# Performance work log

Hardware: AMD Instinct MI355X
Metric: run time of the kernel (lower is better)

Reference implementation:

```python
import jax, jax.numpy as jnp
import numpy as np

LAMB = 0.05
ITERS = 3
EPS = 1e-6


def _l2norm(x):
    return x / jnp.linalg.norm(x, axis=-1, keepdims=True)


def setup_inputs() -> dict:
    key = jax.random.key(0)
    k1, k2, k3, k4 = jax.random.split(key, 4)
    Bi, Bt, R, W, D = 128, 128, 36, 50, 1024
    # region / word features, L2-normalized so fg_sims are cosine similarities
    imgs = _l2norm(jax.random.normal(k1, (Bi, R, D), dtype=jnp.float32))
    caps = _l2norm(jax.random.normal(k2, (Bt, W, D), dtype=jnp.float32))
    # valid lengths; force max so static shapes R, W match int(lens.max())
    img_lens = jax.random.randint(k3, (Bi,), 10, R + 1).astype(jnp.int32)
    img_lens = img_lens.at[0].set(R)
    cap_lens = jax.random.randint(k4, (Bt,), 5, W + 1).astype(jnp.int32)
    cap_lens = cap_lens.at[0].set(W)
    return {"imgs": imgs, "caps": caps, "img_lens": img_lens, "cap_lens": cap_lens}


def _forward(imgs, caps, img_lens, cap_lens):
    Bi, R, D = imgs.shape
    Bt, W, _ = caps.shape
    # fine-grained similarities: [Bi, Bt, R, W]
    fg_sims = jnp.einsum('ird,cwd->icrw', imgs, caps)
    # fine-grained validity mask from lengths
    img_m = (jnp.arange(R)[None, :] < img_lens[:, None])          # [Bi, R]
    cap_m = (jnp.arange(W)[None, :] < cap_lens[:, None])          # [Bt, W]
    mask = (img_m[:, None, :, None] & cap_m[None, :, None, :])    # [Bi, Bt, R, W] bool
    maskf = mask.astype(fg_sims.dtype)

    # _ave_init: uniform marginals over valid rows / cols
    rmask = img_m[:, None, :].astype(fg_sims.dtype) * jnp.ones((1, Bt, 1), fg_sims.dtype)
    r = rmask / rmask.sum(axis=-1, keepdims=True)                 # [Bi, Bt, R]
    cmask = cap_m[None, :, :].astype(fg_sims.dtype) * jnp.ones((Bi, 1, 1), fg_sims.dtype)
    c = cmask / cmask.sum(axis=-1, keepdims=True)                 # [Bi, Bt, W]

    # Sinkhorn-Knopp on cost (1 - fg_sims), masked entries get cost +inf -> P=0
    P = jnp.where(mask, jnp.exp(-(1.0 - fg_sims) / LAMB), 0.0)
    P = P / (P.sum(axis=(-2, -1), keepdims=True) + EPS)
    for _ in range(ITERS):
        u = P.sum(axis=-1) + EPS                                  # [Bi, Bt, R]
        P = P * (r / u)[..., None]
        v = P.sum(axis=-2) + EPS                                  # [Bi, Bt, W]
        P = P * (c / v)[..., None, :]

    sims = (fg_sims * P * maskf).sum(axis=(-2, -1))               # [Bi, Bt]
    return sims


def reference(imgs, caps, img_lens, cap_lens):
    return _forward(imgs, caps, img_lens, cap_lens)
```

## Files before the change

### kernel.cpp

```cpp
#include <hip/hip_runtime.h>
#include <stdint.h>

#define BI 128
#define BT 128
#define RR 36
#define WW 50
#define DD 1024
#define NN 6400
#define SEPS 1e-6f
#define L2E20 28.853900817779268f

typedef __attribute__((ext_vector_type(8))) short short8v;
typedef __attribute__((ext_vector_type(4))) float float4v;
typedef __attribute__((ext_vector_type(2))) unsigned int uint2v;

__device__ __forceinline__ unsigned short f2bf(float f){
  unsigned u = __float_as_uint(f);
  return (unsigned short)((u + 0x7FFFu + ((u >> 16) & 1u)) >> 16);
}

template<int CTRL>
__device__ __forceinline__ int dpp_addi(int x){
  int y = __builtin_amdgcn_mov_dpp(x, CTRL, 0xF, 0xF, true);
  return x + y;
}
__device__ __forceinline__ int iwaveSum(int x){
  x = dpp_addi<0x121>(x);
  x = dpp_addi<0x122>(x);
  x = dpp_addi<0x124>(x);
  x = dpp_addi<0x128>(x);
  {
    uint2v r = __builtin_amdgcn_permlane16_swap((unsigned)x, (unsigned)x, false, false);
    x = (int)r[0] + (int)r[1];
  }
  {
    uint2v r = __builtin_amdgcn_permlane32_swap((unsigned)x, (unsigned)x, false, false);
    x = (int)r[0] + (int)r[1];
  }
  return x;
}
__device__ __forceinline__ int maskedSum128(const int* __restrict__ v,
                                            int lim, int lane){
  const int a = v[2 * lane];
  const int b = v[2 * lane + 1];
  int s = ((2 * lane) < lim ? a : 0) + ((2 * lane + 1) < lim ? b : 0);
  return iwaveSum(s);
}

__global__ __launch_bounds__(256) void gather_cvt_kernel(
    const float* __restrict__ imgs, const float* __restrict__ caps,
    const int* __restrict__ il, const int* __restrict__ cl,
    unsigned short* __restrict__ Ab, unsigned short* __restrict__ Bb,
    int* __restrict__ rowoff, int* __restrict__ coloff){
  const int b = blockIdx.x;
  const int t = threadIdx.x;
  const int lane = t & 63;
  if (b < BI * RR){
    const int i = b / RR, r = b % RR;
    if (r >= il[i]) return;
    const int ro = maskedSum128(il, i, lane);
    if (r == 0 && t == 0) rowoff[i] = ro;
    const float4 v = *(const float4*)(imgs + (size_t)b * DD + t * 4);
    ushort4 o = make_ushort4(f2bf(v.x), f2bf(v.y), f2bf(v.z), f2bf(v.w));
    *(ushort4*)(Ab + (size_t)(ro + r) * DD + t * 4) = o;
  } else {
    const int bb = b - BI * RR;
    const int c = bb / WW, w = bb % WW;
    if (w >= cl[c]) return;
    const int co = maskedSum128(cl, c, lane);
    if (w == 0 && t == 0) coloff[c] = co;
    const float4 v = *(const float4*)(caps + (size_t)bb * DD + t * 4);
    ushort4 o = make_ushort4(f2bf(v.x), f2bf(v.y), f2bf(v.z), f2bf(v.w));
    *(ushort4*)(Bb + (size_t)(co + w) * DD + t * 4) = o;
  }
}

__global__ __launch_bounds__(256) void gemm_kernel(
    const unsigned short* __restrict__ A, const unsigned short* __restrict__ B,
    const int* __restrict__ il, const int* __restrict__ cl,
    float* __restrict__ C){
  __shared__ __align__(16) unsigned char LDS[49152];
  const int tid = threadIdx.x;
  const int lane = tid & 63, wv = tid >> 6;
  const int Mp = __builtin_amdgcn_readfirstlane(maskedSum128(il, BI, lane));
  const int Np = __builtin_amdgcn_readfirstlane(maskedSum128(cl, BT, lane));
  const int nnb = (Np + 127) >> 7;
  const int nact = ((Mp + 127) >> 7) * nnb;
  const int bx = blockIdx.x;
  if (bx >= nact) return;
  const int mb = bx / nnb, nb = bx - mb * nnb;
  const int m0 = mb * 128, n0 = nb * 128;

  const int l15 = lane & 15, lhi = lane >> 4;
  const int wr = wv >> 1, wc = wv & 1;

  const unsigned short* sp[4];
  #pragma unroll
  for (int j = 0; j < 4; j++){
    const int u = j * 256 + tid;
    const int v = u & 511;
    const int sup = v >> 3, slot = v & 7;
    const int sub = slot ^ (sup & 7);
    const int row = sup * 2 + (sub >> 2);
    const int kg  = sub & 3;
    sp[j] = ((u < 512) ? (A + (size_t)(m0 + row) * DD)
                       : (B + (size_t)(n0 + row) * DD)) + kg * 8;
  }

  float4v acc[4][4];
  #pragma unroll
  for (int a1 = 0; a1 < 4; a1++)
    #pragma unroll
    for (int b1 = 0; b1 < 4; b1++)
      acc[a1][b1] = (float4v){0.f, 0.f, 0.f, 0.f};

#define STAGE(BUF, CH) { \
    _Pragma("unroll") \
    for (int j = 0; j < 4; j++) \
      __builtin_amdgcn_global_load_lds( \
          (const __attribute__((address_space(1))) void*)(sp[j] + (CH) * 32), \
          (__attribute__((address_space(3))) void*)(LDS + (BUF) * 16384 + (j * 256 + tid) * 16), \
          16, 0, 0); }

#define LUNIT(row) (((row) >> 1) * 8 + (((((row) & 1) << 2) + lhi) ^ (((row) >> 1) & 7)))

#define COMPUTE(BUF) { \
    short8v af[4], bf[4]; \
    _Pragma("unroll") \
    for (int tr = 0; tr < 4; tr++){ \
      const int row = wr * 64 + tr * 16 + l15; \
      af[tr] = *(const short8v*)(LDS + (BUF) * 16384 + LUNIT(row) * 16); \
    } \
    _Pragma("unroll") \
    for (int tw = 0; tw < 4; tw++){ \
      const int row = wc * 64 + tw * 16 + l15; \
      bf[tw] = *(const short8v*)(LDS + (BUF) * 16384 + 8192 + LUNIT(row) * 16); \
    } \
    _Pragma("unroll") \
    for (int tr = 0; tr < 4; tr++) \
      _Pragma("unroll") \
      for (int tw = 0; tw < 4; tw++) \
        acc[tr][tw] = __builtin_amdgcn_mfma_f32_16x16x32_bf16( \
            af[tr], bf[tw], acc[tr][tw], 0, 0, 0); }

#define WAIT8  asm volatile("s_waitcnt vmcnt(8)" ::: "memory")
#define WAIT4  asm volatile("s_waitcnt vmcnt(4)" ::: "memory")
#define WAIT0  asm volatile("s_waitcnt vmcnt(0)" ::: "memory")
#define BAR    __builtin_amdgcn_s_barrier()

  STAGE(0, 0);
  STAGE(1, 1);
  #pragma unroll 1
  for (int k = 0; k < 10; k++){
    const int c = 3 * k;
    STAGE(2, c + 2); WAIT8; BAR; COMPUTE(0); BAR;
    STAGE(0, c + 3); WAIT8; BAR; COMPUTE(1); BAR;
    STAGE(1, c + 4); WAIT8; BAR; COMPUTE(2); BAR;
  }
  WAIT4; BAR; COMPUTE(0); BAR;
  WAIT0; BAR; COMPUTE(1);

#undef STAGE
#undef LUNIT
#undef COMPUTE
#undef WAIT8
#undef WAIT4
#undef WAIT0
#undef BAR

  #pragma unroll
  for (int tr = 0; tr < 4; tr++)
    #pragma unroll
    for (int tw = 0; tw < 4; tw++)
      #pragma unroll
      for (int j = 0; j < 4; j++){
        int m = m0 + wr * 64 + tr * 16 + lhi * 4 + j;
        int n = n0 + wc * 64 + tw * 16 + l15;
        C[(size_t)m * NN + n] = acc[tr][tw][j];
      }
}

template<int CTRL>
__device__ __forceinline__ float dpp_add(float x){
  int y = __builtin_amdgcn_mov_dpp(__float_as_int(x), CTRL, 0xF, 0xF, true);
  return x + __int_as_float(y);
}
__device__ __forceinline__ float q16sum(float x){
  x = dpp_add<0x121>(x);
  x = dpp_add<0x122>(x);
  x = dpp_add<0x124>(x);
  x = dpp_add<0x128>(x);
  return x;
}
__device__ __forceinline__ float pl16comb(float x){
  unsigned xi = __float_as_uint(x);
  uint2v r = __builtin_amdgcn_permlane16_swap(xi, xi, false, false);
  return __uint_as_float(r[0]) + __uint_as_float(r[1]);
}
__device__ __forceinline__ float pl32comb(float x){
  unsigned xi = __float_as_uint(x);
  uint2v r = __builtin_amdgcn_permlane32_swap(xi, xi, false, false);
  return __uint_as_float(r[0]) + __uint_as_float(r[1]);
}

__global__ __launch_bounds__(256) void sink_kernel(
    const float* __restrict__ fg, const int* __restrict__ il,
    const int* __restrict__ cl, const int* __restrict__ rowoff,
    const int* __restrict__ coloff, float* __restrict__ out){
  const int lane = threadIdx.x & 63;
  const int gw = blockIdx.x * 4 + (threadIdx.x >> 6);
  const int i = gw >> 7, c = gw & 127;
  const int q = lane >> 4, t = lane & 15;

  const int ilen = __builtin_amdgcn_readfirstlane(il[i]);
  const int clen = __builtin_amdgcn_readfirstlane(cl[c]);
  const int ro   = __builtin_amdgcn_readfirstlane(rowoff[i]);
  const int co   = __builtin_amdgcn_readfirstlane(coloff[c]);
  const float* base = fg + (size_t)ro * NN + co;
  const float inv_il = __fdividef(1.0f, (float)ilen);
  const float inv_cl = __fdividef(1.0f, (float)clen);
  const bool v0 = (t      < clen);
  const bool v1 = (t + 16 < clen);
  const bool v2 = (t + 32 < clen);
  const bool v3 = (t + 48 < clen);
  const int r0 = 9 * q;
  const int off0 = r0 * NN + t;

  float p0[9], p1[9], p2[9], p3[9];
  float ts = 0.f;
  #pragma unroll
  for (int k = 0; k < 9; k++){
    const bool rv = (r0 + k) < ilen;
    const float a0 = base[off0 + k * NN];
    const float a1 = base[off0 + k * NN + 16];
    const float a2 = base[off0 + k * NN + 32];
    const float a3 = base[off0 + k * NN + 48];
    p0[k] = (rv && v0) ? exp2f(fmaf(a0, L2E20, -L2E20)) : 0.f;
    p1[k] = (rv && v1) ? exp2f(fmaf(a1, L2E20, -L2E20)) : 0.f;
    p2[k] = (rv && v2) ? exp2f(fmaf(a2, L2E20, -L2E20)) : 0.f;
    p3[k] = (rv && v3) ? exp2f(fmaf(a3, L2E20, -L2E20)) : 0.f;
    ts += (p0[k] + p1[k]) + (p2[k] + p3[k]);
  }
  ts = q16sum(ts);
  ts = pl16comb(ts);
  ts = pl32comb(ts);
  const float sc = __fdividef(1.0f, ts + SEPS);
  #pragma unroll
  for (int k = 0; k < 9; k++){
    p0[k] *= sc; p1[k] *= sc; p2[k] *= sc; p3[k] *= sc;
  }

  for (int it = 0; it < 3; it++){
    #pragma unroll
    for (int k = 0; k < 9; k++){
      float u = (p0[k] + p1[k]) + (p2[k] + p3[k]);
      u = q16sum(u);
      const float rs = __fdividef(inv_il, u + SEPS);
      p0[k] *= rs; p1[k] *= rs; p2[k] *= rs; p3[k] *= rs;
    }
    float s0 = 0.f, s1 = 0.f, s2 = 0.f, s3 = 0.f;
    #pragma unroll
    for (int k = 0; k < 9; k++){
      s0 += p0[k]; s1 += p1[k]; s2 += p2[k]; s3 += p3[k];
    }
    s0 = pl16comb(s0); s0 = pl32comb(s0);
    s1 = pl16comb(s1); s1 = pl32comb(s1);
    s2 = pl16comb(s2); s2 = pl32comb(s2);
    s3 = pl16comb(s3); s3 = pl32comb(s3);
    const float cs0 = __fdividef(inv_cl, s0 + SEPS);
    const float cs1 = __fdividef(inv_cl, s1 + SEPS);
    const float cs2 = __fdividef(inv_cl, s2 + SEPS);
    const float cs3 = __fdividef(inv_cl, s3 + SEPS);
    #pragma unroll
    for (int k = 0; k < 9; k++){
      p0[k] *= cs0; p1[k] *= cs1; p2[k] *= cs2; p3[k] *= cs3;
    }
  }

  float sim = 0.f;
  #pragma unroll
  for (int k = 0; k < 9; k++){
    sim = fmaf(base[off0 + k * NN],      p0[k], sim);
    sim = fmaf(base[off0 + k * NN + 16], p1[k], sim);
    sim = fmaf(base[off0 + k * NN + 32], p2[k], sim);
    sim = fmaf(base[off0 + k * NN + 48], p3[k], sim);
  }
  sim = q16sum(sim);
  sim = pl16comb(sim);
  sim = pl32comb(sim);
  if (lane == 0) out[i * BT + c] = sim;
}

extern "C" void kernel_launch(void* const* d_in, const int* in_sizes, int n_in,
                              void* d_out, int out_size, void* d_ws, size_t ws_size,
                              hipStream_t stream){
  const float* imgs = (const float*)d_in[0];
  const float* caps = (const float*)d_in[1];
  const int* il = (const int*)d_in[2];
  const int* cl = (const int*)d_in[3];
  float* out = (float*)d_out;

  unsigned short* Ab = (unsigned short*)d_ws;
  unsigned short* Bb = Ab + (size_t)BI * RR * DD;
  float* fg = (float*)(Bb + (size_t)BT * WW * DD);
  int* rowoff = (int*)(fg + (size_t)BI * RR * NN);
  int* coloff = rowoff + 128;

  gather_cvt_kernel<<<BI * RR + BT * WW, 256, 0, stream>>>(
      imgs, caps, il, cl, Ab, Bb, rowoff, coloff);
  gemm_kernel<<<36 * 50, 256, 0, stream>>>(Ab, Bb, il, cl, fg);
  sink_kernel<<<(BI * BT) / 4, 256, 0, stream>>>(fg, il, cl, rowoff, coloff, out);
}
```

Measured before the change: 96.15 us.

## Split GEMM K dimension in two and sum partial results in Sinkhorn kernel

Adds a split-K GEMM variant that launches twice as many blocks, each covering half of the K range and writing to its own fp32 output buffer. The Sinkhorn kernel then adds the two partial buffers on load. The aim is more blocks in flight during the GEMM, whose packed tile count is small for the CU count. In exchange, the fp32 intermediate written and read doubles, and the path only runs when the workspace is large enough for a second buffer.

```diff
diff --git a/kernel.cpp b/kernel.cpp
--- a/kernel.cpp
+++ b/kernel.cpp
@@ -75,7 +75,115 @@
   }
 }
 
-__global__ __launch_bounds__(256) void gemm_kernel(
+__global__ __launch_bounds__(256) void gemm16_kernel(
+    const unsigned short* __restrict__ A, const unsigned short* __restrict__ B,
+    const int* __restrict__ il, const int* __restrict__ cl,
+    float* __restrict__ C0, float* __restrict__ C1){
+  __shared__ __align__(16) unsigned char LDS[49152];
+  const int tid = threadIdx.x;
+  const int lane = tid & 63, wv = tid >> 6;
+  const int Mp = __builtin_amdgcn_readfirstlane(maskedSum128(il, BI, lane));
+  const int Np = __builtin_amdgcn_readfirstlane(maskedSum128(cl, BT, lane));
+  const int nnb = (Np + 127) >> 7;
+  const int nact = ((Mp + 127) >> 7) * nnb;
+  const int bx = blockIdx.x;
+  const int tile = bx >> 1;
+  if (tile >= nact) return;
+  const int kh = bx & 1;
+  const int k0 = kh << 4;
+  float* __restrict__ C = kh ? C1 : C0;
+  const int mb = tile / nnb, nb = tile - mb * nnb;
+  const int m0 = mb * 128, n0 = nb * 128;
+
+  const int l15 = lane & 15, lhi = lane >> 4;
+  const int wr = wv >> 1, wc = wv & 1;
+
+  const unsigned short* sp[4];
+  #pragma unroll
+  for (int j = 0; j < 4; j++){
+    const int u = j * 256 + tid;
+    const int v = u & 511;
+    const int sup = v >> 3, slot = v & 7;
+    const int sub = slot ^ (sup & 7);
+    const int row = sup * 2 + (sub >> 2);
+    const int kg  = sub & 3;
+    sp[j] = ((u < 512) ? (A + (size_t)(m0 + row) * DD)
+                       : (B + (size_t)(n0 + row) * DD)) + kg * 8;
+  }
+
+  float4v acc[4][4];
+  #pragma unroll
+  for (int a1 = 0; a1 < 4; a1++)
+    #pragma unroll
+    for (int b1 = 0; b1 < 4; b1++)
+      acc[a1][b1] = (float4v){0.f, 0.f, 0.f, 0.f};
+
+#define STAGE(BUF, CH) { \
+    _Pragma("unroll") \
+    for (int j = 0; j < 4; j++) \
+      __builtin_amdgcn_global_load_lds( \
+          (const __attribute__((address_space(1))) void*)(sp[j] + (CH) * 32), \
+          (__attribute__((address_space(3))) void*)(LDS + (BUF) * 16384 + (j * 256 + tid) * 16), \
+          16, 0, 0); }
+#define LUNIT(row) (((row) >> 1) * 8 + (((((row) & 1) << 2) + lhi) ^ (((row) >> 1) & 7)))
+#define COMPUTE(BUF) { \
+    short8v af[4], bf[4]; \
+    _Pragma("unroll") \
+    for (int tr = 0; tr < 4; tr++){ \
+      const int row = wr * 64 + tr * 16 + l15; \
+      af[tr] = *(const short8v*)(LDS + (BUF) * 16384 + LUNIT(row) * 16); \
+    } \
+    _Pragma("unroll") \
+    for (int tw = 0; tw < 4; tw++){ \
+      const int row = wc * 64 + tw * 16 + l15; \
+      bf[tw] = *(const short8v*)(LDS + (BUF) * 16384 + 8192 + LUNIT(row) * 16); \
+    } \
+    _Pragma("unroll") \
+    for (int tr = 0; tr < 4; tr++) \
+      _Pragma("unroll") \
+      for (int tw = 0; tw < 4; tw++) \
+        acc[tr][tw] = __builtin_amdgcn_mfma_f32_16x16x32_bf16( \
+            af[tr], bf[tw], acc[tr][tw], 0, 0, 0); }
+#define WAIT8  asm volatile("s_waitcnt vmcnt(8)" ::: "memory")
+#define WAIT4  asm volatile("s_waitcnt vmcnt(4)" ::: "memory")
+#define WAIT0  asm volatile("s_waitcnt vmcnt(0)" ::: "memory")
+#define BAR    __builtin_amdgcn_s_barrier()
+
+  STAGE(0, k0 + 0);
+  STAGE(1, k0 + 1);
+  #pragma unroll 1
+  for (int k = 0; k < 4; k++){
+    const int c = k0 + 3 * k;
+    STAGE(2, c + 2); WAIT8; BAR; COMPUTE(0); BAR;
+    STAGE(0, c + 3); WAIT8; BAR; COMPUTE(1); BAR;
+    STAGE(1, c + 4); WAIT8; BAR; COMPUTE(2); BAR;
+  }
+  STAGE(2, k0 + 14); WAIT8; BAR; COMPUTE(0); BAR;
+  STAGE(0, k0 + 15); WAIT8; BAR; COMPUTE(1); BAR;
+  WAIT4; BAR; COMPUTE(2); BAR;
+  WAIT0; BAR; COMPUTE(0);
+
+#undef STAGE
+#undef LUNIT
+#undef COMPUTE
+#undef WAIT8
+#undef WAIT4
+#undef WAIT0
+#undef BAR
+
+  #pragma unroll
+  for (int tr = 0; tr < 4; tr++)
+    #pragma unroll
+    for (int tw = 0; tw < 4; tw++)
+      #pragma unroll
+      for (int j = 0; j < 4; j++){
+        int m = m0 + wr * 64 + tr * 16 + lhi * 4 + j;
+        int n = n0 + wc * 64 + tw * 16 + l15;
+        C[(size_t)m * NN + n] = acc[tr][tw][j];
+      }
+}
+
+__global__ __launch_bounds__(256) void gemm32_kernel(
     const unsigned short* __restrict__ A, const unsigned short* __restrict__ B,
     const int* __restrict__ il, const int* __restrict__ cl,
     float* __restrict__ C){
@@ -90,7 +198,6 @@
   if (bx >= nact) return;
   const int mb = bx / nnb, nb = bx - mb * nnb;
   const int m0 = mb * 128, n0 = nb * 128;
-
   const int l15 = lane & 15, lhi = lane >> 4;
   const int wr = wv >> 1, wc = wv & 1;
 
@@ -121,9 +228,7 @@
           (const __attribute__((address_space(1))) void*)(sp[j] + (CH) * 32), \
           (__attribute__((address_space(3))) void*)(LDS + (BUF) * 16384 + (j * 256 + tid) * 16), \
           16, 0, 0); }
-
 #define LUNIT(row) (((row) >> 1) * 8 + (((((row) & 1) << 2) + lhi) ^ (((row) >> 1) & 7)))
-
 #define COMPUTE(BUF) { \
     short8v af[4], bf[4]; \
     _Pragma("unroll") \
@@ -142,7 +247,6 @@
       for (int tw = 0; tw < 4; tw++) \
         acc[tr][tw] = __builtin_amdgcn_mfma_f32_16x16x32_bf16( \
             af[tr], bf[tw], acc[tr][tw], 0, 0, 0); }
-
 #define WAIT8  asm volatile("s_waitcnt vmcnt(8)" ::: "memory")
 #define WAIT4  asm volatile("s_waitcnt vmcnt(4)" ::: "memory")
 #define WAIT0  asm volatile("s_waitcnt vmcnt(0)" ::: "memory")
@@ -201,6 +305,98 @@
   unsigned xi = __float_as_uint(x);
   uint2v r = __builtin_amdgcn_permlane32_swap(xi, xi, false, false);
   return __uint_as_float(r[0]) + __uint_as_float(r[1]);
+}
+
+__global__ __launch_bounds__(256) void sink_split_kernel(
+    const float* __restrict__ fg, const float* __restrict__ fgb,
+    const int* __restrict__ il, const int* __restrict__ cl,
+    const int* __restrict__ rowoff, const int* __restrict__ coloff,
+    float* __restrict__ out){
+  const int lane = threadIdx.x & 63;
+  const int gw = blockIdx.x * 4 + (threadIdx.x >> 6);
+  const int i = gw >> 7, c = gw & 127;
+  const int q = lane >> 4, t = lane & 15;
+
+  const int ilen = __builtin_amdgcn_readfirstlane(il[i]);
+  const int clen = __builtin_amdgcn_readfirstlane(cl[c]);
+  const int ro   = __builtin_amdgcn_readfirstlane(rowoff[i]);
+  const int co   = __builtin_amdgcn_readfirstlane(coloff[c]);
+  const float* base  = fg  + (size_t)ro * NN + co;
+  const float* base2 = fgb + (size_t)ro * NN + co;
+  const float inv_il = __fdividef(1.0f, (float)ilen);
+  const float inv_cl = __fdividef(1.0f, (float)clen);
+  const bool v0 = (t      < clen);
+  const bool v1 = (t + 16 < clen);
+  const bool v2 = (t + 32 < clen);
+  const bool v3 = (t + 48 < clen);
+  const int r0 = 9 * q;
+  const int off0 = r0 * NN + t;
+
+  float p0[9], p1[9], p2[9], p3[9];
+  float ts = 0.f;
+  #pragma unroll
+  for (int k = 0; k < 9; k++){
+    const bool rv = (r0 + k) < ilen;
+    const int x = off0 + k * NN;
+    const float a0 = base[x]      + base2[x];
+    const float a1 = base[x + 16] + base2[x + 16];
+    const float a2 = base[x + 32] + base2[x + 32];
+    const float a3 = base[x + 48] + base2[x + 48];
+    p0[k] = (rv && v0) ? exp2f(fmaf(a0, L2E20, -L2E20)) : 0.f;
+    p1[k] = (rv && v1) ? exp2f(fmaf(a1, L2E20, -L2E20)) : 0.f;
+    p2[k] = (rv && v2) ? exp2f(fmaf(a2, L2E20, -L2E20)) : 0.f;
+    p3[k] = (rv && v3) ? exp2f(fmaf(a3, L2E20, -L2E20)) : 0.f;
+    ts += (p0[k] + p1[k]) + (p2[k] + p3[k]);
+  }
+  ts = q16sum(ts);
+  ts = pl16comb(ts);
+  ts = pl32comb(ts);
+  const float sc = __fdividef(1.0f, ts + SEPS);
+  #pragma unroll
+  for (int k = 0; k < 9; k++){
+    p0[k] *= sc; p1[k] *= sc; p2[k] *= sc; p3[k] *= sc;
+  }
+
+  for (int it = 0; it < 3; it++){
+    #pragma unroll
+    for (int k = 0; k < 9; k++){
+      float u = (p0[k] + p1[k]) + (p2[k] + p3[k]);
+      u = q16sum(u);
+      const float rs = __fdividef(inv_il, u + SEPS);
+      p0[k] *= rs; p1[k] *= rs; p2[k] *= rs; p3[k] *= rs;
+    }
+    float s0 = 0.f, s1 = 0.f, s2 = 0.f, s3 = 0.f;
+    #pragma unroll
+    for (int k = 0; k < 9; k++){
+      s0 += p0[k]; s1 += p1[k]; s2 += p2[k]; s3 += p3[k];
+    }
+    s0 = pl16comb(s0); s0 = pl32comb(s0);
+    s1 = pl16comb(s1); s1 = pl32comb(s1);
+    s2 = pl16comb(s2); s2 = pl32comb(s2);
+    s3 = pl16comb(s3); s3 = pl32comb(s3);
+    const float cs0 = __fdividef(inv_cl, s0 + SEPS);
+    const float cs1 = __fdividef(inv_cl, s1 + SEPS);
+    const float cs2 = __fdividef(inv_cl, s2 + SEPS);
+    const float cs3 = __fdividef(inv_cl, s3 + SEPS);
+    #pragma unroll
+    for (int k = 0; k < 9; k++){
+      p0[k] *= cs0; p1[k] *= cs1; p2[k] *= cs2; p3[k] *= cs3;
+    }
+  }
+
+  float sim = 0.f;
+  #pragma unroll
+  for (int k = 0; k < 9; k++){
+    const int x = off0 + k * NN;
+    sim = fmaf(base[x],       p0[k], sim); sim = fmaf(base2[x],      p0[k], sim);
+    sim = fmaf(base[x + 16],  p1[k], sim); sim = fmaf(base2[x + 16], p1[k], sim);
+    sim = fmaf(base[x + 32],  p2[k], sim); sim = fmaf(base2[x + 32], p2[k], sim);
+    sim = fmaf(base[x + 48],  p3[k], sim); sim = fmaf(base2[x + 48], p3[k], sim);
+  }
+  sim = q16sum(sim);
+  sim = pl16comb(sim);
+  sim = pl32comb(sim);
+  if (lane == 0) out[i * BT + c] = sim;
 }
 
 __global__ __launch_bounds__(256) void sink_kernel(
@@ -249,7 +445,6 @@
   for (int k = 0; k < 9; k++){
     p0[k] *= sc; p1[k] *= sc; p2[k] *= sc; p3[k] *= sc;
   }
-
   for (int it = 0; it < 3; it++){
     #pragma unroll
     for (int k = 0; k < 9; k++){
@@ -276,7 +471,6 @@
       p0[k] *= cs0; p1[k] *= cs1; p2[k] *= cs2; p3[k] *= cs3;
     }
   }
-
   float sim = 0.f;
   #pragma unroll
   for (int k = 0; k < 9; k++){
@@ -300,14 +494,27 @@
   const int* cl = (const int*)d_in[3];
   float* out = (float*)d_out;
 
-  unsigned short* Ab = (unsigned short*)d_ws;
+  int* rowoff = (int*)d_ws;
+  int* coloff = rowoff + 128;
+  unsigned short* Ab = (unsigned short*)((char*)d_ws + 1024);
   unsigned short* Bb = Ab + (size_t)BI * RR * DD;
-  float* fg = (float*)(Bb + (size_t)BT * WW * DD);
-  int* rowoff = (int*)(fg + (size_t)BI * RR * NN);
-  int* coloff = rowoff + 128;
+  float* fg  = (float*)(Bb + (size_t)BT * WW * DD);
+  float* fg2 = fg + (size_t)BI * RR * NN;
+
+  const size_t fgBytes = (size_t)BI * RR * NN * 4;
+  const size_t need2 = 1024 + ((size_t)BI * RR + (size_t)BT * WW) * DD * 2
+                       + 2 * fgBytes;
+  const bool split = (ws_size >= need2);
 
   gather_cvt_kernel<<<BI * RR + BT * WW, 256, 0, stream>>>(
       imgs, caps, il, cl, Ab, Bb, rowoff, coloff);
-  gemm_kernel<<<36 * 50, 256, 0, stream>>>(Ab, Bb, il, cl, fg);
-  sink_kernel<<<(BI * BT) / 4, 256, 0, stream>>>(fg, il, cl, rowoff, coloff, out);
-}
+  if (split){
+    gemm16_kernel<<<2 * 36 * 50, 256, 0, stream>>>(Ab, Bb, il, cl, fg, fg2);
+    sink_split_kernel<<<(BI * BT) / 4, 256, 0, stream>>>(
+        fg, fg2, il, cl, rowoff, coloff, out);
+  } else {
+    gemm32_kernel<<<36 * 50, 256, 0, stream>>>(Ab, Bb, il, cl, fg);
+    sink_kernel<<<(BI * BT) / 4, 256, 0, stream>>>(
+        fg, il, cl, rowoff, coloff, out);
+  }
+}
```

Result: slower. 114.3 us (+18.8%).
